# Kernel tuning notes

Hardware: AMD Instinct MI355X
Metric: run time of the kernel (lower is better)

## Reference

```python
import jax, jax.numpy as jnp
import numpy as np
import math

# ---- static configuration (mirrors __init__ kwargs) ----
G, M = 64, 128              # graphs x atoms-per-graph
N = G * M                   # 8192 nodes
NUM_RADIAL = 16
DENSITY_W = 1.0
PROJ_W = np.linspace(0.5, 3.0, NUM_RADIAL)
# e^2/(4*pi*eps0) = 14.3996... eV*Angstrom; FIELD_CONSTANT/(4*pi) is used in the code
FIELD_CONSTANT = 4.0 * np.pi * 14.399645351950548
KC = FIELD_CONSTANT / (4.0 * np.pi)

def _dfact(n):
    return 1 if n <= 1 else n * _dfact(n - 2)

def _cl_sigma(l, s, norm):
    # GTO g_l(r) ~ r^l exp(-r^2/(2 s^2)).
    if norm == 'multipoles':   # unit multipole moment normalization
        return 1.0 / ((2.0 * np.pi) ** 1.5 * s ** (3 + 2 * l) * _dfact(2 * l + 1))
    # 'receiver': L2-normalized radial GTO
    return 1.0 / np.sqrt(np.pi ** 1.5 * s ** (3 + 2 * l) * _dfact(2 * l + 1) / 2.0 ** l)

# buffers (registered in __init__)
TOTAL_W = jnp.asarray(np.sqrt((DENSITY_W ** 2 + PROJ_W ** 2) / 2.0), jnp.float32)          # [S]
L0F = jnp.asarray([_cl_sigma(0, s, 'receiver') / _cl_sigma(0, s, 'multipoles') for s in PROJ_W], jnp.float32)
L1W = jnp.asarray([math.sqrt(3.0) * s * s * _cl_sigma(1, s, 'receiver') / _cl_sigma(0, s, 'multipoles') for s in PROJ_W], jnp.float32)
SQRT_PI = math.sqrt(math.pi)
DIP_IDX = np.array([3, 1, 2])   # source_feats columns -> cartesian dipole (x,y,z)


def setup_inputs() -> dict:
    key = jax.random.key(0)
    k1, k2 = jax.random.split(key)
    source_feats = jax.random.normal(k1, (N, 4), jnp.float32) * 0.5       # [q, mu_y, mu_z, mu_x]
    node_positions = jax.random.uniform(k2, (N, 3), jnp.float32) * 12.0   # Angstrom box
    batch = jnp.asarray(np.repeat(np.arange(G), M), jnp.int32)
    # per-graph complete directed graph without self loops (matches the torch helper with N=1)
    base = np.arange(M)
    row = np.repeat(base, M); col = np.tile(base, M)
    keep = row != col
    row, col = row[keep], col[keep]
    off = (np.arange(G) * M)[:, None]
    sender = (row[None, :] + off).reshape(-1)
    receiver = (col[None, :] + off).reshape(-1)
    edge_index = jnp.asarray(np.stack([sender, receiver]), jnp.int32)     # [2, E]
    return {"source_feats": source_feats, "node_positions": node_positions,
            "batch": batch, "edge_index": edge_index}


def _forward(source_feats, node_positions, edge_index):
    n_nodes = node_positions.shape[0]
    S = NUM_RADIAL
    sender, receiver = edge_index[0], edge_index[1]
    R = node_positions[receiver] - node_positions[sender]          # [E,3]
    r = jnp.linalg.norm(R, axis=-1)
    r_e = jnp.maximum(r, 1e-10)[:, None]                           # [E,1]
    Rhat = R / r_e                                                 # [E,3]
    w = TOTAL_W[None, :]                                           # [1,S]
    g_s = jnp.exp(-r_e ** 2 / (4.0 * w ** 2)) / (w * SQRT_PI)      # [E,S]
    T_s = jax.scipy.special.erf(r_e / (2.0 * w)) / r_e             # [E,S]
    fp_s = (g_s - T_s) / r_e                                       # [E,S]
    q_j = source_feats[sender, 0]                                  # [E]
    mu_j = source_feats[sender][:, DIP_IDX]                        # [E,3]
    mu_Rhat = jnp.sum(mu_j * Rhat, axis=-1)                        # [E]
    # l=0 channels
    contrib_l0 = q_j[:, None] * T_s - mu_Rhat[:, None] * fp_s      # [E,S]
    feat_l0 = jax.ops.segment_sum(contrib_l0, receiver, num_segments=n_nodes)
    feat_l0 = KC * L0F[None, :] * feat_l0                          # [N,S]
    # l=1 channels
    fp_over_r = fp_s / r_e
    fpp_s = -g_s / (2.0 * w ** 2) - 2.0 * g_s / r_e ** 2 + 2.0 * T_s / r_e ** 2
    contrib_l1 = fp_s[..., None] * Rhat[:, None, :] * q_j[:, None, None]              # [E,S,3]
    contrib_l1 = contrib_l1 - fp_over_r[..., None] * mu_j[:, None, :]
    contrib_l1 = contrib_l1 + ((fp_over_r - fpp_s) * mu_Rhat[:, None])[..., None] * Rhat[:, None, :]
    E = contrib_l1.shape[0]
    feat_l1 = jax.ops.segment_sum(contrib_l1.reshape(E, -1), receiver, num_segments=n_nodes)
    feat_l1 = KC * L1W[None, :, None] * feat_l1.reshape(n_nodes, S, 3)                # [N,S,3]
    # output layout: [l0 (S) | interleaved (y,z,x) per radial (3S)]
    out_l1 = feat_l1[:, :, np.array([1, 2, 0])].reshape(n_nodes, 3 * S)
    features = jnp.concatenate([feat_l0, out_l1], axis=1)                             # [N,4S]
    # GTO self-interaction (r -> 0 analytic limits): T(0)=1/(w sqrt(pi)), fp(0)=0,
    # fp_over_r(0) = -1/(6 w^3 sqrt(pi)), fp_over_r(0)-fpp(0) = 0.
    q = source_feats[:, 0]
    si_l0 = KC * L0F[None, :] * q[:, None] / (TOTAL_W[None, :] * SQRT_PI)             # [N,S]
    mu = source_feats[:, DIP_IDX]                                                     # [N,3]
    si_coef = KC * L1W / (6.0 * TOTAL_W ** 3 * SQRT_PI)                               # [S]
    si_l1 = si_coef[None, :, None] * mu[:, None, np.array([1, 2, 0])]                 # [N,S,3] in (y,z,x)
    si_terms = jnp.concatenate([si_l0, si_l1.reshape(n_nodes, 3 * S)], axis=1)        # [N,4S]
    return features, si_terms


def reference(source_feats, node_positions, batch, edge_index):
    # batch only determines edge_index (precomputed statically in setup_inputs)
    features, si_terms = _forward(source_feats, node_positions, edge_index)
    # include_self_interaction=False -> features returned unmodified; module returns (features, si_terms, None)
    return (features, si_terms)
```

## Files before the change

kernel.cpp:

```cpp
#include <hip/hip_runtime.h>
#include <math.h>

#define NNODES 8192
#define MNODES 128
#define NS 16
#define RPB 16
#define BLOCK (RPB*8)

struct Coefs {
  float inv2w[NS];
  float c1[NS];
  float inv2w2[NS];
  float sl0[NS];
  float sl1[NS];
  float si0[NS];
  float si1[NS];
};

__global__ __launch_bounds__(BLOCK)
void elec_feat_kernel(const float* __restrict__ feats,
                      const float* __restrict__ pos,
                      float* __restrict__ out,
                      Coefs C)
{
  __shared__ float spx[MNODES], spy[MNODES], spz[MNODES];
  __shared__ float sq[MNODES], sm0[MNODES], sm1[MNODES], sm2[MNODES];
  __shared__ __align__(16) float sfeat[RPB * 64];
  __shared__ __align__(16) float ssi[RPB * 64];

  const int tid = threadIdx.x;
  const int g = blockIdx.x >> 3;
  const int rbase = (blockIdx.x & 7) * RPB;
  const int nodebase = g * MNODES;

  {
    const int n = nodebase + tid;
    const float4 f = reinterpret_cast<const float4*>(feats)[n];
    sq[tid] = f.x; sm0[tid] = f.w; sm1[tid] = f.y; sm2[tid] = f.z;
    spx[tid] = pos[3 * n + 0];
    spy[tid] = pos[3 * n + 1];
    spz[tid] = pos[3 * n + 2];
  }
  __syncthreads();

  const int chunk = tid & 7;
  const int rsub = tid >> 3;
  const int rl = rbase + rsub;

  const float rx = spx[rl], ry = spy[rl], rz = spz[rl];

  float a0[NS], ax[NS], ay[NS], az[NS];
#pragma unroll
  for (int s = 0; s < NS; ++s) { a0[s] = 0.f; ax[s] = 0.f; ay[s] = 0.f; az[s] = 0.f; }

  for (int k = 0; k < MNODES / 8; ++k) {
    const int j = (k << 3) | chunk;
    if (j == rl) continue;
    const float Rx = rx - spx[j], Ry = ry - spy[j], Rz = rz - spz[j];
    float r2 = fmaf(Rx, Rx, fmaf(Ry, Ry, Rz * Rz));
    r2 = fmaxf(r2, 1e-20f);
    const float inv_r = __builtin_amdgcn_rsqf(r2);
    const float r = r2 * inv_r;
    const float inv_r2 = inv_r * inv_r;
    const float hx = Rx * inv_r, hy = Ry * inv_r, hz = Rz * inv_r;
    const float qj = sq[j];
    const float m0 = sm0[j], m1 = sm1[j], m2 = sm2[j];
    const float muR = fmaf(m0, hx, fmaf(m1, hy, m2 * hz));
#pragma unroll
    for (int s = 0; s < NS; ++s) {
      const float x = r * C.inv2w[s];
      const float e = __builtin_amdgcn_exp2f(-1.4426950408889634f * x * x);
      const float gs = C.c1[s] * e;
      const float t = __builtin_amdgcn_rcpf(fmaf(0.3275911f, x, 1.0f));
      float p = fmaf(1.061405429f, t, -1.453152027f);
      p = fmaf(p, t, 1.421413741f);
      p = fmaf(p, t, -0.284496736f);
      p = fmaf(p, t, 0.254829592f);
      p = p * t;
      const float erfv = fmaf(-p, e, 1.0f);
      const float T = erfv * inv_r;
      const float fp = (gs - T) * inv_r;
      const float fpr = fp * inv_r;
      const float fpp = fmaf(-gs, C.inv2w2[s], 2.0f * inv_r2 * (T - gs));
      a0[s] = fmaf(qj, T, fmaf(-muR, fp, a0[s]));
      const float ca = fmaf(fpr - fpp, muR, fp * qj);
      ax[s] = fmaf(ca, hx, fmaf(-fpr, m0, ax[s]));
      ay[s] = fmaf(ca, hy, fmaf(-fpr, m1, ay[s]));
      az[s] = fmaf(ca, hz, fmaf(-fpr, m2, az[s]));
    }
  }

#pragma unroll
  for (int s = 0; s < NS; ++s) {
#pragma unroll
    for (int m = 1; m < 8; m <<= 1) {
      a0[s] += __shfl_xor(a0[s], m);
      ax[s] += __shfl_xor(ax[s], m);
      ay[s] += __shfl_xor(ay[s], m);
      az[s] += __shfl_xor(az[s], m);
    }
  }

  if (chunk == 0) {
    float* F = &sfeat[rsub * 64];
    float* Si = &ssi[rsub * 64];
#pragma unroll
    for (int s = 0; s < NS; ++s) F[s] = C.sl0[s] * a0[s];
#pragma unroll
    for (int s = 0; s < NS; ++s) {
      F[16 + 3 * s + 0] = C.sl1[s] * ay[s];
      F[16 + 3 * s + 1] = C.sl1[s] * az[s];
      F[16 + 3 * s + 2] = C.sl1[s] * ax[s];
    }
    const float qr = sq[rl];
    const float f1 = sm1[rl], f2 = sm2[rl], f3 = sm0[rl];
#pragma unroll
    for (int s = 0; s < NS; ++s) Si[s] = C.si0[s] * qr;
#pragma unroll
    for (int s = 0; s < NS; ++s) {
      Si[16 + 3 * s + 0] = C.si1[s] * f1;
      Si[16 + 3 * s + 1] = C.si1[s] * f2;
      Si[16 + 3 * s + 2] = C.si1[s] * f3;
    }
  }
  __syncthreads();

  const size_t i0 = (size_t)(nodebase + rbase);
  float4* df = reinterpret_cast<float4*>(out + i0 * 64);
  float4* ds = reinterpret_cast<float4*>(out + (size_t)NNODES * 64 + i0 * 64);
  const float4* lf = reinterpret_cast<const float4*>(sfeat);
  const float4* ls = reinterpret_cast<const float4*>(ssi);
  df[tid] = lf[tid];
  df[tid + BLOCK] = lf[tid + BLOCK];
  ds[tid] = ls[tid];
  ds[tid + BLOCK] = ls[tid + BLOCK];
}

extern "C" void kernel_launch(void* const* d_in, const int* in_sizes, int n_in,
                              void* d_out, int out_size, void* d_ws, size_t ws_size,
                              hipStream_t stream) {
  const float* feats = (const float*)d_in[0];
  const float* pos = (const float*)d_in[1];
  float* out = (float*)d_out;

  Coefs C;
  const double KC = 14.399645351950548;
  const double SP = sqrt(M_PI);
  for (int s = 0; s < NS; ++s) {
    const double sig = 0.5 + (double)s * (2.5 / 15.0);
    const double w = sqrt((1.0 + sig * sig) * 0.5);
    const double cl0m = 1.0 / (pow(2.0 * M_PI, 1.5) * pow(sig, 3.0));
    const double cl0r = 1.0 / sqrt(pow(M_PI, 1.5) * pow(sig, 3.0));
    const double cl1r = 1.0 / sqrt(pow(M_PI, 1.5) * pow(sig, 5.0) * 1.5);
    const double L0F = cl0r / cl0m;
    const double L1W = sqrt(3.0) * sig * sig * cl1r / cl0m;
    C.inv2w[s]  = (float)(1.0 / (2.0 * w));
    C.c1[s]     = (float)(1.0 / (w * SP));
    C.inv2w2[s] = (float)(1.0 / (2.0 * w * w));
    C.sl0[s]    = (float)(KC * L0F);
    C.sl1[s]    = (float)(KC * L1W);
    C.si0[s]    = (float)(KC * L0F / (w * SP));
    C.si1[s]    = (float)(KC * L1W / (6.0 * w * w * w * SP));
  }

  hipLaunchKernelGGL(elec_feat_kernel, dim3(NNODES / RPB), dim3(BLOCK), 0, stream,
                     feats, pos, out, C);
}
```

Before: 87.43 us.

## Pack radial channels into float2 vectors, double chunk parallelism, constexpr coefficient table

Processes pairs of radial channels as float2 vectors so the compiler can emit packed FP32 math, and doubles the block to 16 chunks per receiver so each thread handles 8 senders instead of 16. It computes coefficients at compile time instead of passing a kernel argument struct, packs positions and charges into float4 shared arrays, and replaces the branch on self pairs with masking. It also moves the constant exp scale into the table and uses r2 directly in the exponent. The trade-offs are an extra shuffle-reduction stage, a slightly different r2 clamp, and register pressure that could limit occupancy under the bound of 2 blocks.

```diff
diff --git a/kernel.cpp b/kernel.cpp
--- a/kernel.cpp
+++ b/kernel.cpp
@@ -1,30 +1,58 @@
 #include <hip/hip_runtime.h>
-#include <math.h>
 
 #define NNODES 8192
 #define MNODES 128
 #define NS 16
+#define NP 8
 #define RPB 16
-#define BLOCK (RPB*8)
+#define CHUNKS 16
+#define BLOCK (RPB*CHUNKS)
 
-struct Coefs {
-  float inv2w[NS];
-  float c1[NS];
-  float inv2w2[NS];
-  float sl0[NS];
-  float sl1[NS];
-  float si0[NS];
-  float si1[NS];
+typedef float v2f __attribute__((ext_vector_type(2)));
+
+constexpr double csqrt_(double x) {
+  double g = x > 1.0 ? x : 1.0;
+  for (int i = 0; i < 100; ++i) g = 0.5 * (g + x / g);
+  return g;
+}
+
+struct CTab {
+  float inv2w[NS], cexp[NS], c1[NS], i2w2[NS], sl0[NS], sl1[NS], si0[NS], si1[NS];
+  constexpr CTab() : inv2w{}, cexp{}, c1{}, i2w2{}, sl0{}, sl1{}, si0{}, si1{} {
+    const double PI = 3.14159265358979323846;
+    const double KC = 14.399645351950548;
+    const double SP = csqrt_(PI);
+    const double p2pi15 = 2.0 * PI * csqrt_(2.0 * PI);
+    const double pi15 = PI * csqrt_(PI);
+    for (int s = 0; s < NS; ++s) {
+      const double sig = 0.5 + s * (2.5 / 15.0);
+      const double w = csqrt_((1.0 + sig * sig) * 0.5);
+      const double s3 = sig * sig * sig;
+      const double cl0m = 1.0 / (p2pi15 * s3);
+      const double cl0r = 1.0 / csqrt_(pi15 * s3);
+      const double cl1r = 1.0 / csqrt_(pi15 * s3 * sig * sig * 1.5);
+      const double L0F = cl0r / cl0m;
+      const double L1W = csqrt_(3.0) * sig * sig * cl1r / cl0m;
+      inv2w[s] = (float)(0.5 / w);
+      cexp[s]  = (float)(-1.4426950408889634 * 0.25 / (w * w));
+      c1[s]    = (float)(1.0 / (w * SP));
+      i2w2[s]  = (float)(0.5 / (w * w));
+      sl0[s]   = (float)(KC * L0F);
+      sl1[s]   = (float)(KC * L1W);
+      si0[s]   = (float)(KC * L0F / (w * SP));
+      si1[s]   = (float)(KC * L1W / (6.0 * w * w * w * SP));
+    }
+  }
 };
+constexpr CTab CT{};
 
-__global__ __launch_bounds__(BLOCK)
+__global__ __launch_bounds__(BLOCK, 2)
 void elec_feat_kernel(const float* __restrict__ feats,
                       const float* __restrict__ pos,
-                      float* __restrict__ out,
-                      Coefs C)
+                      float* __restrict__ out)
 {
-  __shared__ float spx[MNODES], spy[MNODES], spz[MNODES];
-  __shared__ float sq[MNODES], sm0[MNODES], sm1[MNODES], sm2[MNODES];
+  __shared__ __align__(16) float4 spq[MNODES];
+  __shared__ __align__(16) float4 smu[MNODES];
   __shared__ __align__(16) float sfeat[RPB * 64];
   __shared__ __align__(16) float ssi[RPB * 64];
 
@@ -33,71 +61,87 @@
   const int rbase = (blockIdx.x & 7) * RPB;
   const int nodebase = g * MNODES;
 
-  {
+  if (tid < MNODES) {
     const int n = nodebase + tid;
     const float4 f = reinterpret_cast<const float4*>(feats)[n];
-    sq[tid] = f.x; sm0[tid] = f.w; sm1[tid] = f.y; sm2[tid] = f.z;
-    spx[tid] = pos[3 * n + 0];
-    spy[tid] = pos[3 * n + 1];
-    spz[tid] = pos[3 * n + 2];
+    spq[tid] = make_float4(pos[3 * n], pos[3 * n + 1], pos[3 * n + 2], f.x);
+    smu[tid] = make_float4(f.w, f.y, f.z, 0.f);
   }
   __syncthreads();
 
-  const int chunk = tid & 7;
-  const int rsub = tid >> 3;
+  const int chunk = tid & (CHUNKS - 1);
+  const int rsub = tid >> 4;
   const int rl = rbase + rsub;
 
-  const float rx = spx[rl], ry = spy[rl], rz = spz[rl];
+  const float4 rp = spq[rl];
 
-  float a0[NS], ax[NS], ay[NS], az[NS];
+  v2f A0[NP], AX[NP], AY[NP], AZ[NP];
 #pragma unroll
-  for (int s = 0; s < NS; ++s) { a0[s] = 0.f; ax[s] = 0.f; ay[s] = 0.f; az[s] = 0.f; }
+  for (int p = 0; p < NP; ++p) {
+    A0[p] = (v2f){0.f, 0.f}; AX[p] = (v2f){0.f, 0.f};
+    AY[p] = (v2f){0.f, 0.f}; AZ[p] = (v2f){0.f, 0.f};
+  }
 
-  for (int k = 0; k < MNODES / 8; ++k) {
-    const int j = (k << 3) | chunk;
-    if (j == rl) continue;
-    const float Rx = rx - spx[j], Ry = ry - spy[j], Rz = rz - spz[j];
+  for (int k = 0; k < MNODES / CHUNKS; ++k) {
+    const int j = (k << 4) | chunk;
+    const float4 sp = spq[j];
+    const float4 sm = smu[j];
+    const bool self = (j == rl);
+    const float Rx = rp.x - sp.x, Ry = rp.y - sp.y, Rz = rp.z - sp.z;
     float r2 = fmaf(Rx, Rx, fmaf(Ry, Ry, Rz * Rz));
-    r2 = fmaxf(r2, 1e-20f);
+    r2 = fmaxf(r2, 1e-12f);
     const float inv_r = __builtin_amdgcn_rsqf(r2);
     const float r = r2 * inv_r;
-    const float inv_r2 = inv_r * inv_r;
+    const float tir2 = 2.f * inv_r * inv_r;
     const float hx = Rx * inv_r, hy = Ry * inv_r, hz = Rz * inv_r;
-    const float qj = sq[j];
-    const float m0 = sm0[j], m1 = sm1[j], m2 = sm2[j];
+    const float qj = self ? 0.f : sp.w;
+    const float m0 = self ? 0.f : sm.x;
+    const float m1 = self ? 0.f : sm.y;
+    const float m2 = self ? 0.f : sm.z;
     const float muR = fmaf(m0, hx, fmaf(m1, hy, m2 * hz));
+
 #pragma unroll
-    for (int s = 0; s < NS; ++s) {
-      const float x = r * C.inv2w[s];
-      const float e = __builtin_amdgcn_exp2f(-1.4426950408889634f * x * x);
-      const float gs = C.c1[s] * e;
-      const float t = __builtin_amdgcn_rcpf(fmaf(0.3275911f, x, 1.0f));
-      float p = fmaf(1.061405429f, t, -1.453152027f);
-      p = fmaf(p, t, 1.421413741f);
-      p = fmaf(p, t, -0.284496736f);
-      p = fmaf(p, t, 0.254829592f);
-      p = p * t;
-      const float erfv = fmaf(-p, e, 1.0f);
-      const float T = erfv * inv_r;
-      const float fp = (gs - T) * inv_r;
-      const float fpr = fp * inv_r;
-      const float fpp = fmaf(-gs, C.inv2w2[s], 2.0f * inv_r2 * (T - gs));
-      a0[s] = fmaf(qj, T, fmaf(-muR, fp, a0[s]));
-      const float ca = fmaf(fpr - fpp, muR, fp * qj);
-      ax[s] = fmaf(ca, hx, fmaf(-fpr, m0, ax[s]));
-      ay[s] = fmaf(ca, hy, fmaf(-fpr, m1, ay[s]));
-      az[s] = fmaf(ca, hz, fmaf(-fpr, m2, az[s]));
+    for (int p = 0; p < NP; ++p) {
+      const v2f cI = {CT.inv2w[2 * p], CT.inv2w[2 * p + 1]};
+      const v2f cE = {CT.cexp[2 * p],  CT.cexp[2 * p + 1]};
+      const v2f cC = {CT.c1[2 * p],    CT.c1[2 * p + 1]};
+      const v2f cW = {CT.i2w2[2 * p],  CT.i2w2[2 * p + 1]};
+      const v2f ea = cE * r2;
+      v2f e;
+      e.x = __builtin_amdgcn_exp2f(ea.x);
+      e.y = __builtin_amdgcn_exp2f(ea.y);
+      const v2f x = cI * r;
+      const v2f ta = 0.3275911f * x + 1.0f;
+      v2f t;
+      t.x = __builtin_amdgcn_rcpf(ta.x);
+      t.y = __builtin_amdgcn_rcpf(ta.y);
+      v2f pp = 1.061405429f * t - 1.453152027f;
+      pp = pp * t + 1.421413741f;
+      pp = pp * t - 0.284496736f;
+      pp = pp * t + 0.254829592f;
+      pp = pp * t;
+      const v2f erfv = 1.0f - pp * e;
+      const v2f T = erfv * inv_r;
+      const v2f gs = cC * e;
+      const v2f fp = (gs - T) * inv_r;
+      const v2f fpr = fp * inv_r;
+      const v2f fpp = (T - gs) * tir2 - gs * cW;
+      A0[p] += qj * T - muR * fp;
+      const v2f ca = (fpr - fpp) * muR + fp * qj;
+      AX[p] += ca * hx - fpr * m0;
+      AY[p] += ca * hy - fpr * m1;
+      AZ[p] += ca * hz - fpr * m2;
     }
   }
 
 #pragma unroll
-  for (int s = 0; s < NS; ++s) {
+  for (int p = 0; p < NP; ++p) {
 #pragma unroll
-    for (int m = 1; m < 8; m <<= 1) {
-      a0[s] += __shfl_xor(a0[s], m);
-      ax[s] += __shfl_xor(ax[s], m);
-      ay[s] += __shfl_xor(ay[s], m);
-      az[s] += __shfl_xor(az[s], m);
+    for (int m = 1; m < CHUNKS; m <<= 1) {
+      A0[p].x += __shfl_xor(A0[p].x, m); A0[p].y += __shfl_xor(A0[p].y, m);
+      AX[p].x += __shfl_xor(AX[p].x, m); AX[p].y += __shfl_xor(AX[p].y, m);
+      AY[p].x += __shfl_xor(AY[p].x, m); AY[p].y += __shfl_xor(AY[p].y, m);
+      AZ[p].x += __shfl_xor(AZ[p].x, m); AZ[p].y += __shfl_xor(AZ[p].y, m);
     }
   }
 
@@ -105,22 +149,25 @@
     float* F = &sfeat[rsub * 64];
     float* Si = &ssi[rsub * 64];
 #pragma unroll
-    for (int s = 0; s < NS; ++s) F[s] = C.sl0[s] * a0[s];
+    for (int s = 0; s < NS; ++s) {
+      const int p = s >> 1, c = s & 1;
+      const float a0 = c ? A0[p].y : A0[p].x;
+      const float axv = c ? AX[p].y : AX[p].x;
+      const float ayv = c ? AY[p].y : AY[p].x;
+      const float azv = c ? AZ[p].y : AZ[p].x;
+      F[s] = CT.sl0[s] * a0;
+      F[16 + 3 * s + 0] = CT.sl1[s] * ayv;
+      F[16 + 3 * s + 1] = CT.sl1[s] * azv;
+      F[16 + 3 * s + 2] = CT.sl1[s] * axv;
+    }
+    const float qr = spq[rl].w;
+    const float4 mr = smu[rl];
 #pragma unroll
     for (int s = 0; s < NS; ++s) {
-      F[16 + 3 * s + 0] = C.sl1[s] * ay[s];
-      F[16 + 3 * s + 1] = C.sl1[s] * az[s];
-      F[16 + 3 * s + 2] = C.sl1[s] * ax[s];
-    }
-    const float qr = sq[rl];
-    const float f1 = sm1[rl], f2 = sm2[rl], f3 = sm0[rl];
-#pragma unroll
-    for (int s = 0; s < NS; ++s) Si[s] = C.si0[s] * qr;
-#pragma unroll
-    for (int s = 0; s < NS; ++s) {
-      Si[16 + 3 * s + 0] = C.si1[s] * f1;
-      Si[16 + 3 * s + 1] = C.si1[s] * f2;
-      Si[16 + 3 * s + 2] = C.si1[s] * f3;
+      Si[s] = CT.si0[s] * qr;
+      Si[16 + 3 * s + 0] = CT.si1[s] * mr.y;
+      Si[16 + 3 * s + 1] = CT.si1[s] * mr.z;
+      Si[16 + 3 * s + 2] = CT.si1[s] * mr.x;
     }
   }
   __syncthreads();
@@ -128,12 +175,8 @@
   const size_t i0 = (size_t)(nodebase + rbase);
   float4* df = reinterpret_cast<float4*>(out + i0 * 64);
   float4* ds = reinterpret_cast<float4*>(out + (size_t)NNODES * 64 + i0 * 64);
-  const float4* lf = reinterpret_cast<const float4*>(sfeat);
-  const float4* ls = reinterpret_cast<const float4*>(ssi);
-  df[tid] = lf[tid];
-  df[tid + BLOCK] = lf[tid + BLOCK];
-  ds[tid] = ls[tid];
-  ds[tid + BLOCK] = ls[tid + BLOCK];
+  df[tid] = reinterpret_cast<const float4*>(sfeat)[tid];
+  ds[tid] = reinterpret_cast<const float4*>(ssi)[tid];
 }
 
 extern "C" void kernel_launch(void* const* d_in, const int* in_sizes, int n_in,
@@ -142,27 +185,6 @@
   const float* feats = (const float*)d_in[0];
   const float* pos = (const float*)d_in[1];
   float* out = (float*)d_out;
-
-  Coefs C;
-  const double KC = 14.399645351950548;
-  const double SP = sqrt(M_PI);
-  for (int s = 0; s < NS; ++s) {
-    const double sig = 0.5 + (double)s * (2.5 / 15.0);
-    const double w = sqrt((1.0 + sig * sig) * 0.5);
-    const double cl0m = 1.0 / (pow(2.0 * M_PI, 1.5) * pow(sig, 3.0));
-    const double cl0r = 1.0 / sqrt(pow(M_PI, 1.5) * pow(sig, 3.0));
-    const double cl1r = 1.0 / sqrt(pow(M_PI, 1.5) * pow(sig, 5.0) * 1.5);
-    const double L0F = cl0r / cl0m;
-    const double L1W = sqrt(3.0) * sig * sig * cl1r / cl0m;
-    C.inv2w[s]  = (float)(1.0 / (2.0 * w));
-    C.c1[s]     = (float)(1.0 / (w * SP));
-    C.inv2w2[s] = (float)(1.0 / (2.0 * w * w));
-    C.sl0[s]    = (float)(KC * L0F);
-    C.sl1[s]    = (float)(KC * L1W);
-    C.si0[s]    = (float)(KC * L0F / (w * SP));
-    C.si1[s]    = (float)(KC * L1W / (6.0 * w * w * w * SP));
-  }
-
   hipLaunchKernelGGL(elec_feat_kernel, dim3(NNODES / RPB), dim3(BLOCK), 0, stream,
-                     feats, pos, out, C);
+                     feats, pos, out);
 }
```

New measurement: 78.63 us. -10.1%, faster.
